# Performance work log

Measured on AMD Instinct MI355X. Metric: run time of the kernel, lower is better.

## Reference

```python
import jax, jax.numpy as jnp
import numpy as np
from math import sqrt

B, LQ, LK = 4, 256, 50000
EDGE_IN, NODE_IN, OUT = 128, 128, 256
KV_IN = NODE_IN + EDGE_IN  # 256


def setup_inputs() -> dict:
    key = jax.random.key(0)
    ks = jax.random.split(key, 8)
    s = 0.05
    return {
        "query": jax.random.normal(ks[0], (B, LQ, EDGE_IN), jnp.float32),
        "input": jax.random.normal(ks[1], (B, LK, KV_IN), jnp.float32),
        "Wq": jax.random.normal(ks[2], (OUT, EDGE_IN), jnp.float32) * s,
        "bq": jax.random.normal(ks[3], (OUT,), jnp.float32) * s,
        "Wk": jax.random.normal(ks[4], (OUT, KV_IN), jnp.float32) * s,
        "bk": jax.random.normal(ks[5], (OUT,), jnp.float32) * s,
        "Wv": jax.random.normal(ks[6], (OUT, KV_IN), jnp.float32) * s,
        "bv": jax.random.normal(ks[7], (OUT,), jnp.float32) * s,
    }


def reference(query, input, Wq, bq, Wk, bk, Wv, bv):
    norm = 1.0 / sqrt(OUT)
    Q = query @ Wq.T + bq            # [B, LQ, OUT]
    K = input @ Wk.T + bk            # [B, LK, OUT]
    V = input @ Wv.T + bv            # [B, LK, OUT]
    alpha = jnp.einsum("bqd,bkd->bqk", Q, K) * norm  # [B, LQ, LK]
    alpha = jax.nn.softmax(alpha, axis=-1)
    # z = alpha^T * V broadcasts only because LQ == OUT:
    # out[b, j] = sum_k alpha[b, j, k] * V[b, k, j]
    return jnp.einsum("bqk,bkq->bq", alpha, V)      # [B, OUT]
```

## Files before the change

kernel.cpp:

```cpp
#include <hip/hip_runtime.h>
#include <hip/hip_bf16.h>
#include <stdint.h>

using f32x4  = __attribute__((ext_vector_type(4))) float;
using f32x16 = __attribute__((ext_vector_type(16))) float;
using bf16x8 = __attribute__((ext_vector_type(8))) short;

constexpr int BATCH = 4;
constexpr int LQ_   = 256;
constexpr int LK_   = 50000;
constexpr int OUTD  = 256;
constexpr int EIN   = 128;
constexpr int KB    = 64;
constexpr int NKB   = (LK_ + KB - 1) / KB;
constexpr int BPB   = 64;

__device__ __forceinline__ uint32_t f2bf(float f) {
  uint32_t u = __builtin_bit_cast(uint32_t, f);
  u = (u + 0x7fffu + ((u >> 16) & 1u)) >> 16;
  return u;
}

__global__ __launch_bounds__(256) void prep_all(
    const float* __restrict__ query, const float* __restrict__ Wq,
    const float* __restrict__ bq,    const float* __restrict__ Wk,
    const float* __restrict__ Wv,    ushort* __restrict__ Gn,
    ushort* __restrict__ Wvbf,       float* __restrict__ numden)
{
  const int blk = blockIdx.x, tid = threadIdx.x;
  if (blk >= 64) {
    if (blk < 96) {
      int base = (blk - 64) * 2048 + tid * 8;
      float4 a = *(const float4*)(Wv + base);
      float4 c = *(const float4*)(Wv + base + 4);
      uint4 pk;
      pk.x = f2bf(a.x) | (f2bf(a.y) << 16);
      pk.y = f2bf(a.z) | (f2bf(a.w) << 16);
      pk.z = f2bf(c.x) | (f2bf(c.y) << 16);
      pk.w = f2bf(c.z) | (f2bf(c.w) << 16);
      *(uint4*)(Wvbf + base) = pk;
    } else {
      for (int i = tid; i < 2 * BATCH * OUTD; i += 256) numden[i] = 0.f;
    }
    return;
  }
  __shared__ float qin[16 * EIN];
  __shared__ float Qr [16 * OUTD];
  const int b = blk >> 4, q0 = (blk & 15) * 16;
  {
    int idx = tid * 8;
    int row = idx >> 7, c = idx & 127;
    const float* p = query + ((size_t)b * LQ_ + q0 + row) * EIN + c;
    float4 a = *(const float4*)p;
    float4 d = *(const float4*)(p + 4);
    float* q = &qin[row * EIN + c];
    q[0]=a.x; q[1]=a.y; q[2]=a.z; q[3]=a.w; q[4]=d.x; q[5]=d.y; q[6]=d.z; q[7]=d.w;
  }
  __syncthreads();

  float acc[16];
  {
    float bias = bq[tid];
#pragma unroll
    for (int i = 0; i < 16; ++i) acc[i] = bias;
  }
  for (int d4 = 0; d4 < EIN / 4; ++d4) {
    f32x4 w4 = *(const f32x4*)(Wq + tid * EIN + d4 * 4);
#pragma unroll
    for (int i = 0; i < 16; ++i) {
      f32x4 q4 = *(const f32x4*)(qin + i * EIN + d4 * 4);
      acc[i] += q4[0]*w4[0] + q4[1]*w4[1] + q4[2]*w4[2] + q4[3]*w4[3];
    }
  }
#pragma unroll
  for (int i = 0; i < 16; ++i) Qr[i * OUTD + tid] = acc[i];
  __syncthreads();

  float acc2[16];
#pragma unroll
  for (int i = 0; i < 16; ++i) acc2[i] = 0.f;
  for (int d4 = 0; d4 < OUTD / 4; ++d4) {
    float w0 = Wk[(d4*4+0) * OUTD + tid];
    float w1 = Wk[(d4*4+1) * OUTD + tid];
    float w2 = Wk[(d4*4+2) * OUTD + tid];
    float w3 = Wk[(d4*4+3) * OUTD + tid];
#pragma unroll
    for (int i = 0; i < 16; ++i) {
      f32x4 q4 = *(const f32x4*)(Qr + i * OUTD + d4 * 4);
      acc2[i] += q4[0]*w0 + q4[1]*w1 + q4[2]*w2 + q4[3]*w3;
    }
  }
  const float norm = 0.0625f;
#pragma unroll
  for (int i = 0; i < 16; ++i)
    Gn[((size_t)b * LQ_ + q0 + i) * OUTD + tid] = (ushort)f2bf(acc2[i] * norm);
}

__global__ __launch_bounds__(512, 2) void attn_main(
    const float*  __restrict__ input, const ushort* __restrict__ Gn,
    const ushort* __restrict__ Wvbf,  float* __restrict__ num,
    float* __restrict__ den)
{
  __shared__ ushort lds[2 * 16384];
  const int b = blockIdx.x >> 6, blk = blockIdx.x & (BPB - 1);
  const int t0 = (blk * NKB) >> 6, t1 = ((blk + 1) * NKB) >> 6;
  const int tid = threadIdx.x, w = tid >> 6, l = tid & 63;
  const float* src = input + (size_t)b * LK_ * 256;

  const int arow = w * 32 + (l & 31);
  const int hi = l >> 5;
  const ushort* gp = Gn   + ((size_t)b * LQ_ + arow) * 256 + hi * 8;
  const ushort* vp = Wvbf + (size_t)arow * 256 + hi * 8;
  bf16x8 ga[16], wa[16];
#pragma unroll
  for (int k = 0; k < 16; ++k) {
    ga[k] = *(const bf16x8*)(gp + k * 16);
    wa[k] = *(const bf16x8*)(vp + k * 16);
  }

  float numr[16], denr[16];
#pragma unroll
  for (int r = 0; r < 16; ++r) { numr[r] = 0.f; denr[r] = 0.f; }

  float4 rga[4], rgb[4];
  auto loadreg = [&](int t) {
#pragma unroll
    for (int i = 0; i < 4; ++i) {
      int g = i * 512 + tid;
      int row = t * KB + (g >> 5);
      row = row < LK_ ? row : LK_ - 1;
      const float* p = src + (size_t)row * 256 + (g & 31) * 8;
      rga[i] = *(const float4*)p;
      rgb[i] = *(const float4*)(p + 4);
    }
  };
  auto writebuf = [&](int buf) {
    char* base = (char*)lds + buf * 32768;
#pragma unroll
    for (int i = 0; i < 4; ++i) {
      int g = i * 512 + tid;
      int row = g >> 5, fb = g & 31;
      uint4 pk;
      pk.x = f2bf(rga[i].x) | (f2bf(rga[i].y) << 16);
      pk.y = f2bf(rga[i].z) | (f2bf(rga[i].w) << 16);
      pk.z = f2bf(rgb[i].x) | (f2bf(rgb[i].y) << 16);
      pk.w = f2bf(rgb[i].z) | (f2bf(rgb[i].w) << 16);
      *(uint4*)(base + fb * 1024 + ((row ^ (fb & 7)) * 16)) = pk;
    }
  };

  loadreg(t0);
  writebuf(0);
  if (t0 + 1 < t1) loadreg(t0 + 1);
  __syncthreads();

  for (int t = t0; t < t1; ++t) {
    const int p = (t - t0) & 1;
    if (t + 1 < t1) {
      writebuf(p ^ 1);
      if (t + 2 < t1) loadreg(t + 2);
    }
    const char* base = (const char*)lds + p * 32768;

#pragma unroll 1
    for (int ct = 0; ct < 2; ++ct) {
      f32x16 aS = {0,0,0,0,0,0,0,0,0,0,0,0,0,0,0,0};
      f32x16 aV = {0,0,0,0,0,0,0,0,0,0,0,0,0,0,0,0};
      const int r = ct * 32 + (l & 31);
#pragma unroll
      for (int ks = 0; ks < 16; ++ks) {
        const int fb = ks * 2 + hi;
        bf16x8 bb = *(const bf16x8*)(base + fb * 1024 + ((r ^ (fb & 7)) * 16));
        aS = __builtin_amdgcn_mfma_f32_32x32x16_bf16(ga[ks], bb, aS, 0, 0, 0);
        aV = __builtin_amdgcn_mfma_f32_32x32x16_bf16(wa[ks], bb, aV, 0, 0, 0);
      }
      const int krow = t * KB + r;
      const bool valid = krow < LK_;
#pragma unroll
      for (int rr = 0; rr < 16; ++rr) {
        float e = valid ? __expf(aS[rr]) : 0.f;
        denr[rr] += e;
        numr[rr] += e * aV[rr];
      }
    }
    __syncthreads();
  }

#pragma unroll
  for (int r = 0; r < 16; ++r) {
    float d_ = denr[r], n_ = numr[r];
#pragma unroll
    for (int m = 1; m < 32; m <<= 1) {
      d_ += __shfl_xor(d_, m, 64);
      n_ += __shfl_xor(n_, m, 64);
    }
    if ((l & 31) == 0) {
      int q = w * 32 + (r & 3) + 8 * (r >> 2) + 4 * hi;
      atomicAdd(&den[b * OUTD + q], d_);
      atomicAdd(&num[b * OUTD + q], n_);
    }
  }
}

__global__ __launch_bounds__(256) void finalize(const float* __restrict__ num,
                                                const float* __restrict__ den,
                                                const float* __restrict__ bv,
                                                float* __restrict__ out) {
  int i = blockIdx.x * 256 + threadIdx.x;
  out[i] = num[i] / den[i] + bv[i & 255];
}

extern "C" void kernel_launch(void* const* d_in, const int* in_sizes, int n_in,
                              void* d_out, int out_size, void* d_ws, size_t ws_size,
                              hipStream_t stream)
{
  const float* query = (const float*)d_in[0];
  const float* input = (const float*)d_in[1];
  const float* Wq    = (const float*)d_in[2];
  const float* bq    = (const float*)d_in[3];
  const float* Wk    = (const float*)d_in[4];
  const float* Wv    = (const float*)d_in[6];
  const float* bv    = (const float*)d_in[7];
  float* out = (float*)d_out;

  char* ws = (char*)d_ws;
  ushort* Gn     = (ushort*)ws;
  ushort* Wvbf   = (ushort*)(ws + 524288);
  float*  numden = (float*)(ws + 524288 + 131072);
  float*  num    = numden;
  float*  den    = numden + BATCH * OUTD;

  prep_all<<<97, 256, 0, stream>>>(query, Wq, bq, Wk, Wv, Gn, Wvbf, numden);
  attn_main<<<BATCH * BPB, 512, 0, stream>>>(input, Gn, Wvbf, num, den);
  finalize<<<BATCH, 256, 0, stream>>>(num, den, bv, out);
}
```

Measured before the change: 118.6 us.

## Split score and value MFMA work across separate waves with LDS exp exchange

Doubles the block to 1024 threads and gives the score GEMM (Gn·K) and the value GEMM (Wv·K) to separate groups of 8 waves, so each wave holds only one A-fragment set. Score waves compute exp and write it to a shared LDS tile, and value waves read it to accumulate the numerator. The key tile shrinks from 64 to 32 rows per iteration, with a simpler swizzle. The aim is to cut per-wave register pressure and raise occupancy so the bandwidth-bound streaming of the input hides latency better. The cost is an extra barrier per tile and LDS traffic for the exp values. loadreg(t0+1) now runs unconditionally, relying on row clamping.

```diff
diff --git a/kernel.cpp b/kernel.cpp
--- a/kernel.cpp
+++ b/kernel.cpp
@@ -11,8 +11,8 @@
 constexpr int LK_   = 50000;
 constexpr int OUTD  = 256;
 constexpr int EIN   = 128;
-constexpr int KB    = 64;
-constexpr int NKB   = (LK_ + KB - 1) / KB;
+constexpr int TKB   = 32;
+constexpr int NKT   = (LK_ + TKB - 1) / TKB;
 constexpr int BPB   = 64;
 
 __device__ __forceinline__ uint32_t f2bf(float f) {
@@ -96,108 +96,109 @@
     Gn[((size_t)b * LQ_ + q0 + i) * OUTD + tid] = (ushort)f2bf(acc2[i] * norm);
 }
 
-__global__ __launch_bounds__(512, 2) void attn_main(
+__global__ __launch_bounds__(1024, 4) void attn_main(
     const float*  __restrict__ input, const ushort* __restrict__ Gn,
     const ushort* __restrict__ Wvbf,  float* __restrict__ num,
     float* __restrict__ den)
 {
-  __shared__ ushort lds[2 * 16384];
+  __shared__ ushort bb[2 * 8192];
+  __shared__ float  etile[8192];
   const int b = blockIdx.x >> 6, blk = blockIdx.x & (BPB - 1);
-  const int t0 = (blk * NKB) >> 6, t1 = ((blk + 1) * NKB) >> 6;
+  const int t0 = (blk * NKT) >> 6, t1 = ((blk + 1) * NKT) >> 6;
   const int tid = threadIdx.x, w = tid >> 6, l = tid & 63;
+  const int wq = w & 7;
+  const bool isS = (w < 8);
+  const int hi = l >> 5, lk = l & 31;
   const float* src = input + (size_t)b * LK_ * 256;
 
-  const int arow = w * 32 + (l & 31);
-  const int hi = l >> 5;
-  const ushort* gp = Gn   + ((size_t)b * LQ_ + arow) * 256 + hi * 8;
-  const ushort* vp = Wvbf + (size_t)arow * 256 + hi * 8;
-  bf16x8 ga[16], wa[16];
-#pragma unroll
-  for (int k = 0; k < 16; ++k) {
-    ga[k] = *(const bf16x8*)(gp + k * 16);
-    wa[k] = *(const bf16x8*)(vp + k * 16);
-  }
-
-  float numr[16], denr[16];
-#pragma unroll
-  for (int r = 0; r < 16; ++r) { numr[r] = 0.f; denr[r] = 0.f; }
-
-  float4 rga[4], rgb[4];
+  const int arow = wq * 32 + lk;
+  const ushort* ap = (isS ? (Gn + ((size_t)b * LQ_ + arow) * 256)
+                          : (Wvbf + (size_t)arow * 256)) + hi * 8;
+  bf16x8 af[16];
+#pragma unroll
+  for (int k = 0; k < 16; ++k) af[k] = *(const bf16x8*)(ap + k * 16);
+
+  float accR[16];
+#pragma unroll
+  for (int r = 0; r < 16; ++r) accR[r] = 0.f;
+
+  float4 sA0, sA1;
   auto loadreg = [&](int t) {
-#pragma unroll
-    for (int i = 0; i < 4; ++i) {
-      int g = i * 512 + tid;
-      int row = t * KB + (g >> 5);
-      row = row < LK_ ? row : LK_ - 1;
-      const float* p = src + (size_t)row * 256 + (g & 31) * 8;
-      rga[i] = *(const float4*)p;
-      rgb[i] = *(const float4*)(p + 4);
-    }
+    int row = t * TKB + (tid >> 5);
+    row = row < LK_ ? row : LK_ - 1;
+    const float* p = src + (size_t)row * 256 + (tid & 31) * 8;
+    sA0 = *(const float4*)p;
+    sA1 = *(const float4*)(p + 4);
   };
   auto writebuf = [&](int buf) {
-    char* base = (char*)lds + buf * 32768;
-#pragma unroll
-    for (int i = 0; i < 4; ++i) {
-      int g = i * 512 + tid;
-      int row = g >> 5, fb = g & 31;
-      uint4 pk;
-      pk.x = f2bf(rga[i].x) | (f2bf(rga[i].y) << 16);
-      pk.y = f2bf(rga[i].z) | (f2bf(rga[i].w) << 16);
-      pk.z = f2bf(rgb[i].x) | (f2bf(rgb[i].y) << 16);
-      pk.w = f2bf(rgb[i].z) | (f2bf(rgb[i].w) << 16);
-      *(uint4*)(base + fb * 1024 + ((row ^ (fb & 7)) * 16)) = pk;
-    }
+    int fb = tid & 31, row = tid >> 5;
+    uint4 pk;
+    pk.x = f2bf(sA0.x) | (f2bf(sA0.y) << 16);
+    pk.y = f2bf(sA0.z) | (f2bf(sA0.w) << 16);
+    pk.z = f2bf(sA1.x) | (f2bf(sA1.y) << 16);
+    pk.w = f2bf(sA1.z) | (f2bf(sA1.w) << 16);
+    *(uint4*)((char*)bb + buf * 16384 + fb * 512 + ((row ^ fb) * 16)) = pk;
   };
 
   loadreg(t0);
   writebuf(0);
-  if (t0 + 1 < t1) loadreg(t0 + 1);
+  loadreg(t0 + 1);
   __syncthreads();
+
+  char* emy = (char*)etile + wq * 4096 + l * 16;
 
   for (int t = t0; t < t1; ++t) {
     const int p = (t - t0) & 1;
+    const char* base = (const char*)bb + p * 16384;
+
+    f32x16 aX = {0,0,0,0,0,0,0,0,0,0,0,0,0,0,0,0};
+#pragma unroll
+    for (int ks = 0; ks < 16; ++ks) {
+      const int fb = ks * 2 + hi;
+      bf16x8 bv = *(const bf16x8*)(base + fb * 512 + ((lk ^ fb) * 16));
+      aX = __builtin_amdgcn_mfma_f32_32x32x16_bf16(af[ks], bv, aX, 0, 0, 0);
+    }
+
+    if (isS) {
+      const bool valid = (t * TKB + lk) < LK_;
+#pragma unroll
+      for (int r4 = 0; r4 < 4; ++r4) {
+        f32x4 ev;
+#pragma unroll
+        for (int j = 0; j < 4; ++j) {
+          float e = valid ? __expf(aX[r4 * 4 + j]) : 0.f;
+          ev[j] = e;
+          accR[r4 * 4 + j] += e;
+        }
+        *(f32x4*)(emy + r4 * 1024) = ev;
+      }
+    }
+    __syncthreads();
+
+    if (!isS) {
+#pragma unroll
+      for (int r4 = 0; r4 < 4; ++r4) {
+        f32x4 ev = *(const f32x4*)(emy + r4 * 1024);
+#pragma unroll
+        for (int j = 0; j < 4; ++j)
+          accR[r4 * 4 + j] += ev[j] * aX[r4 * 4 + j];
+      }
+    }
     if (t + 1 < t1) {
       writebuf(p ^ 1);
-      if (t + 2 < t1) loadreg(t + 2);
-    }
-    const char* base = (const char*)lds + p * 32768;
-
-#pragma unroll 1
-    for (int ct = 0; ct < 2; ++ct) {
-      f32x16 aS = {0,0,0,0,0,0,0,0,0,0,0,0,0,0,0,0};
-      f32x16 aV = {0,0,0,0,0,0,0,0,0,0,0,0,0,0,0,0};
-      const int r = ct * 32 + (l & 31);
-#pragma unroll
-      for (int ks = 0; ks < 16; ++ks) {
-        const int fb = ks * 2 + hi;
-        bf16x8 bb = *(const bf16x8*)(base + fb * 1024 + ((r ^ (fb & 7)) * 16));
-        aS = __builtin_amdgcn_mfma_f32_32x32x16_bf16(ga[ks], bb, aS, 0, 0, 0);
-        aV = __builtin_amdgcn_mfma_f32_32x32x16_bf16(wa[ks], bb, aV, 0, 0, 0);
-      }
-      const int krow = t * KB + r;
-      const bool valid = krow < LK_;
-#pragma unroll
-      for (int rr = 0; rr < 16; ++rr) {
-        float e = valid ? __expf(aS[rr]) : 0.f;
-        denr[rr] += e;
-        numr[rr] += e * aV[rr];
-      }
+      loadreg(t + 2);
     }
     __syncthreads();
   }
 
 #pragma unroll
   for (int r = 0; r < 16; ++r) {
-    float d_ = denr[r], n_ = numr[r];
-#pragma unroll
-    for (int m = 1; m < 32; m <<= 1) {
-      d_ += __shfl_xor(d_, m, 64);
-      n_ += __shfl_xor(n_, m, 64);
-    }
-    if ((l & 31) == 0) {
-      int q = w * 32 + (r & 3) + 8 * (r >> 2) + 4 * hi;
-      atomicAdd(&den[b * OUTD + q], d_);
-      atomicAdd(&num[b * OUTD + q], n_);
+    float v = accR[r];
+#pragma unroll
+    for (int m = 1; m < 32; m <<= 1) v += __shfl_xor(v, m, 64);
+    if (lk == 0) {
+      int q = wq * 32 + 4 * hi + (r & 3) + 8 * (r >> 2);
+      atomicAdd((isS ? den : num) + b * OUTD + q, v);
     }
   }
 }
@@ -231,6 +232,6 @@
   float*  den    = numden + BATCH * OUTD;
 
   prep_all<<<97, 256, 0, stream>>>(query, Wq, bq, Wk, Wv, Gn, Wvbf, numden);
-  attn_main<<<BATCH * BPB, 512, 0, stream>>>(input, Gn, Wvbf, num, den);
+  attn_main<<<BATCH * BPB, 1024, 0, stream>>>(input, Gn, Wvbf, num, den);
   finalize<<<BATCH, 256, 0, stream>>>(num, den, bv, out);
 }
```

Measured after the change: 224.9 us. 1.9x slower.
